# Optimization experiments

Measured on AMD Instinct MI355X. Metric: run time of the kernel, lower is better.

Reference implementation:

```python
import jax, jax.numpy as jnp
import numpy as np

N = 100000   # nodes
E = 800000   # edges (avg degree ~8)
G = 64       # graphs in batch
F_IN = 64
H = 128
C = 4


def setup_inputs() -> dict:
    key = jax.random.key(0)
    ks = jax.random.split(key, 14)
    def w(k, fin, fout):
        return jax.random.normal(k, (fin, fout), dtype=jnp.float32) * (1.0 / np.sqrt(fin))
    inp = {
        "x": jax.random.normal(ks[0], (N, F_IN), dtype=jnp.float32),
        "W1": w(ks[1], F_IN, H), "b1": jnp.zeros((H,), jnp.float32),
        "W2": w(ks[2], H, H),    "b2": jnp.zeros((H,), jnp.float32),
        "W3": w(ks[3], H, H),    "b3": jnp.zeros((H,), jnp.float32),
        "fw1": w(ks[4], H, H),   "fb1": jnp.zeros((H,), jnp.float32),
        "fw2": w(ks[5], H, C),   "fb2": jnp.zeros((C,), jnp.float32),
        "edge_index": jax.random.randint(ks[6], (2, E), 0, N, dtype=jnp.int32),
        "batch": jnp.sort(jax.random.randint(ks[7], (N,), 0, G, dtype=jnp.int32)),
    }
    return inp


def gcn_conv(x, W, b, src, dst):
    """PyG GCNConv: linear transform, add self-loops, symmetric deg^-1/2 norm, scatter-add."""
    h = x @ W                                                    # [N, H]
    deg = jax.ops.segment_sum(jnp.ones((E,), x.dtype), dst, num_segments=N) + 1.0  # self-loop
    dinv = jax.lax.rsqrt(deg)                                    # [N]
    norm = dinv[src] * dinv[dst]                                 # [E]
    agg = jax.ops.segment_sum(h[src] * norm[:, None], dst, num_segments=N)
    agg = agg + h * (dinv * dinv)[:, None]                       # self-loop term (norm = 1/deg)
    return agg + b


def reference(x, W1, b1, W2, b2, W3, b3, fw1, fb1, fw2, fb2, edge_index, batch):
    src, dst = edge_index[0], edge_index[1]
    h = jax.nn.relu(gcn_conv(x, W1, b1, src, dst))
    h = jax.nn.relu(gcn_conv(h, W2, b2, src, dst))
    h = gcn_conv(h, W3, b3, src, dst)
    # global mean pool over graphs
    s = jax.ops.segment_sum(h, batch, num_segments=G)            # [G, H]
    cnt = jax.ops.segment_sum(jnp.ones((N,), h.dtype), batch, num_segments=G)
    pooled = s / jnp.maximum(cnt, 1.0)[:, None]
    z = jax.nn.relu(pooled @ fw1 + fb1)
    return z @ fw2 + fb2                                          # [G, C]
```

## Files before the change

### kernel.cpp

```cpp
#include <hip/hip_runtime.h>

#define N_NODES 100000
#define N_EDGES 800000
#define G_GRAPHS 64
#define F_INPUT 64
#define H_DIM 128
#define C_OUT 4
#define CSR_CAP 32
#define EDGE_BLOCKS (N_EDGES / 256)
#define CONV_BLOCKS ((N_NODES + 255) / 256)
#define WPACK_BLOCKS 20
#define FILL_SEG 4
#define FILL_CHUNKS 250
#define FILL_RANGE (N_NODES / FILL_SEG)
#define FILL_CHUNK (N_EDGES / FILL_CHUNKS)
#define FILL_BLOCKS (FILL_SEG * FILL_CHUNKS)
#define SEG_SPAN (FILL_RANGE * CSR_CAP)

typedef __attribute__((ext_vector_type(8))) short bf16x8;
typedef __attribute__((ext_vector_type(8))) unsigned short u16x8;
typedef __attribute__((ext_vector_type(4))) float f32x4;

__device__ inline unsigned short f2bf(float f) {
    union { float f; unsigned int u; } v; v.f = f;
    unsigned int u = v.u + 0x7FFFu + ((v.u >> 16) & 1u);
    return (unsigned short)(u >> 16);
}
__device__ inline float bf2f(unsigned short b) {
    union { unsigned int u; float f; } v; v.u = ((unsigned int)b) << 16;
    return v.f;
}
__device__ inline float2 unpack_pair(unsigned int u) {
    union { unsigned int u; float f; } a, b;
    a.u = u << 16; b.u = u & 0xFFFF0000u;
    float2 r; r.x = a.f; r.y = b.f; return r;
}
__device__ inline unsigned char f2fp8(float v) {
    int r = __builtin_amdgcn_cvt_pk_fp8_f32(v, 0.0f, 0, false);
    return (unsigned char)(r & 0xFF);
}

__device__ inline void wpack_one(const float* __restrict__ W, unsigned short* __restrict__ hi,
                                 unsigned short* __restrict__ lo, int K, int t)
{
    int lane = t & 63;
    int tile = t >> 6;
    int KS = K / 32;
    int ct = tile / KS, ks = tile % KS;
    int n  = ct * 16 + (lane & 15);
    int k0 = ks * 32 + (lane >> 4) * 8;
    #pragma unroll
    for (int j = 0; j < 8; j++) {
        float w = W[(k0 + j) * H_DIM + n];
        unsigned short h = f2bf(w);
        hi[t * 8 + j] = h;
        lo[t * 8 + j] = f2bf(w - bf2f(h));
    }
}

__global__ __launch_bounds__(256) void hist_kernel(
    const int* __restrict__ dst, int* __restrict__ cnt, int* __restrict__ paddr,
    const float* __restrict__ W1, const float* __restrict__ W2, const float* __restrict__ W3,
    unsigned short* __restrict__ w1hi, unsigned short* __restrict__ w1lo,
    unsigned short* __restrict__ w2hi, unsigned short* __restrict__ w2lo,
    unsigned short* __restrict__ w3hi, unsigned short* __restrict__ w3lo)
{
    int b = blockIdx.x;
    if (b < EDGE_BLOCKS) {
        int e = b * 256 + threadIdx.x;
        int d = dst[e];
        int sl = atomicAdd(&cnt[d], 1);
        paddr[e] = (sl < CSR_CAP) ? d * CSR_CAP + sl : -1;
        return;
    }
    b -= EDGE_BLOCKS;
    int t = b * 256 + threadIdx.x;
    if (t < 1024)       wpack_one(W1, w1hi, w1lo, F_INPUT, t);
    else if (t < 3072)  wpack_one(W2, w2hi, w2lo, H_DIM, t - 1024);
    else                wpack_one(W3, w3hi, w3lo, H_DIM, t - 3072);
}

__global__ __launch_bounds__(256) void prep_kernel(
    const int* __restrict__ paddr, const int* __restrict__ src,
    int* __restrict__ csr,
    const int* __restrict__ cnti, const float4* __restrict__ x4,
    float* __restrict__ dinv, unsigned int* __restrict__ xb_u,
    unsigned int* __restrict__ p1z, unsigned int* __restrict__ p3z)
{
    int b = blockIdx.x;
    if (b < FILL_BLOCKS) {
        const int r   = b & (FILL_SEG - 1);
        const int m   = b >> 2;
        const int plo = r * SEG_SPAN;
        const int phi = plo + SEG_SPAN;
        const int e0  = m * FILL_CHUNK;
        for (int e = e0 + threadIdx.x; e < e0 + FILL_CHUNK; e += 256) {
            int pa = paddr[e];
            if (pa >= plo && pa < phi)
                csr[pa] = src[e];
        }
        return;
    }
    b -= FILL_BLOCKS;
    __shared__ float dl[256];
    int i = b * 256 + threadIdx.x;
    float dv = 0.0f;
    if (i < N_NODES) {
        int c  = cnti[i];
        int dc = min(c, CSR_CAP);
        dv = rsqrtf((float)c + 1.0f);
        dinv[i] = dv;
        int pad = (dc + 7) & ~7;
        for (int s2 = dc; s2 < pad; s2++)
            csr[(size_t)i * CSR_CAP + s2] = N_NODES;
    } else if (i == N_NODES) {
        for (int c = 0; c < 32; c++) {
            xb_u[(size_t)N_NODES * 32 + c] = 0u;
            p1z [(size_t)N_NODES * 32 + c] = 0u;
            p3z [(size_t)N_NODES * 32 + c] = 0u;
        }
    }
    dl[threadIdx.x] = dv;
    __syncthreads();
    const int row_base = b * 256;
    for (int c = threadIdx.x; c < 256 * 16; c += 256) {
        int r = c >> 4;
        int row = row_base + r;
        if (row < N_NODES) {
            float d2 = dl[r];
            float4 v = x4[(size_t)row * 16 + (c & 15)];
            size_t o = ((size_t)row * 16 + (c & 15)) * 2;
            xb_u[o + 0] = (unsigned int)f2bf(v.x * d2) | ((unsigned int)f2bf(v.y * d2) << 16);
            xb_u[o + 1] = (unsigned int)f2bf(v.z * d2) | ((unsigned int)f2bf(v.w * d2) << 16);
        }
    }
}

__global__ __launch_bounds__(256) void gather1_kernel(
    const unsigned int* __restrict__ xb_u, const int* __restrict__ cnti,
    const int* __restrict__ csr, const float* __restrict__ dinv,
    unsigned int* __restrict__ outb)
{
    int idx = blockIdx.x * 256 + threadIdx.x;
    int i  = idx >> 5;
    int f2 = idx & 31;
    int dc = min(cnti[i], CSR_CAP);
    int beg  = i * CSR_CAP;
    int end8 = beg + ((dc + 7) & ~7);
    float2 acc = unpack_pair(xb_u[(size_t)i * 32 + f2]);
    for (int e = beg; e < end8; e += 8) {
        int4 c0 = *(const int4*)(csr + e);
        int4 c1 = *(const int4*)(csr + e + 4);
        float2 v0 = unpack_pair(xb_u[(size_t)c0.x * 32 + f2]);
        float2 v1 = unpack_pair(xb_u[(size_t)c0.y * 32 + f2]);
        float2 v2 = unpack_pair(xb_u[(size_t)c0.z * 32 + f2]);
        float2 v3 = unpack_pair(xb_u[(size_t)c0.w * 32 + f2]);
        float2 v4 = unpack_pair(xb_u[(size_t)c1.x * 32 + f2]);
        float2 v5 = unpack_pair(xb_u[(size_t)c1.y * 32 + f2]);
        float2 v6 = unpack_pair(xb_u[(size_t)c1.z * 32 + f2]);
        float2 v7 = unpack_pair(xb_u[(size_t)c1.w * 32 + f2]);
        acc.x += ((v0.x + v1.x) + (v2.x + v3.x)) + ((v4.x + v5.x) + (v6.x + v7.x));
        acc.y += ((v0.y + v1.y) + (v2.y + v3.y)) + ((v4.y + v5.y) + (v6.y + v7.y));
    }
    float dv = dinv[i];
    outb[idx] = (unsigned int)f2bf(acc.x * dv) | ((unsigned int)f2bf(acc.y * dv) << 16);
}

__device__ inline void acc_u2(uint2 w, float* __restrict__ a) {
    auto l0 = __builtin_amdgcn_cvt_pk_f32_fp8(w.x, false);
    auto h0 = __builtin_amdgcn_cvt_pk_f32_fp8(w.x, true);
    auto l1 = __builtin_amdgcn_cvt_pk_f32_fp8(w.y, false);
    auto h1 = __builtin_amdgcn_cvt_pk_f32_fp8(w.y, true);
    a[0] += l0[0]; a[1] += l0[1]; a[2] += h0[0]; a[3] += h0[1];
    a[4] += l1[0]; a[5] += l1[1]; a[6] += h1[0]; a[7] += h1[1];
}
__device__ inline void gather_fp8_u2(
    const uint2* __restrict__ base, const int* __restrict__ csr,
    int i, int beg, int end8, float* __restrict__ a)
{
    acc_u2(base[(size_t)i * 16], a);
    for (int e = beg; e < end8; e += 8) {
        int4 c0 = *(const int4*)(csr + e);
        int4 c1 = *(const int4*)(csr + e + 4);
        uint2 w0 = base[(size_t)c0.x * 16];
        uint2 w1 = base[(size_t)c0.y * 16];
        uint2 w2 = base[(size_t)c0.z * 16];
        uint2 w3 = base[(size_t)c0.w * 16];
        uint2 w4 = base[(size_t)c1.x * 16];
        uint2 w5 = base[(size_t)c1.y * 16];
        uint2 w6 = base[(size_t)c1.z * 16];
        uint2 w7 = base[(size_t)c1.w * 16];
        acc_u2(w0, a); acc_u2(w1, a); acc_u2(w2, a); acc_u2(w3, a);
        acc_u2(w4, a); acc_u2(w5, a); acc_u2(w6, a); acc_u2(w7, a);
    }
}

__global__ __launch_bounds__(256) void gather2_kernel(
    const uint2* __restrict__ hs8, const int* __restrict__ cnti,
    const int* __restrict__ csr, const float* __restrict__ dinv,
    const float* __restrict__ bias, uint2* __restrict__ out8)
{
    int idx = blockIdx.x * 256 + threadIdx.x;
    int i  = idx >> 4;
    int f8 = idx & 15;
    int dc = min(cnti[i], CSR_CAP);
    int beg  = i * CSR_CAP;
    int end8 = beg + ((dc + 7) & ~7);
    float a[8] = {0, 0, 0, 0, 0, 0, 0, 0};
    gather_fp8_u2(hs8 + f8, csr, i, beg, end8, a);
    float dv = dinv[i];
    float4 b0 = *(const float4*)(bias + f8 * 8);
    float4 b1 = *(const float4*)(bias + f8 * 8 + 4);
    float v0 = fmaxf(a[0] * dv + b0.x, 0.0f);
    float v1 = fmaxf(a[1] * dv + b0.y, 0.0f);
    float v2 = fmaxf(a[2] * dv + b0.z, 0.0f);
    float v3 = fmaxf(a[3] * dv + b0.w, 0.0f);
    float v4 = fmaxf(a[4] * dv + b1.x, 0.0f);
    float v5 = fmaxf(a[5] * dv + b1.y, 0.0f);
    float v6 = fmaxf(a[6] * dv + b1.z, 0.0f);
    float v7 = fmaxf(a[7] * dv + b1.w, 0.0f);
    int d0 = __builtin_amdgcn_cvt_pk_fp8_f32(v0, v1, 0, false);
    d0 = __builtin_amdgcn_cvt_pk_fp8_f32(v2, v3, d0, true);
    int d1 = __builtin_amdgcn_cvt_pk_fp8_f32(v4, v5, 0, false);
    d1 = __builtin_amdgcn_cvt_pk_fp8_f32(v6, v7, d1, true);
    uint2 o; o.x = (unsigned int)d0; o.y = (unsigned int)d1;
    out8[(size_t)i * 16 + f8] = o;
}

__global__ __launch_bounds__(256) void gather3_kernel(
    const uint2* __restrict__ hs8, const int* __restrict__ cnti,
    const int* __restrict__ csr, const float* __restrict__ dinv,
    const float* __restrict__ bias, uint4* __restrict__ outb)
{
    int idx = blockIdx.x * 256 + threadIdx.x;
    int i  = idx >> 4;
    int f8 = idx & 15;
    int dc = min(cnti[i], CSR_CAP);
    int beg  = i * CSR_CAP;
    int end8 = beg + ((dc + 7) & ~7);
    float a[8] = {0, 0, 0, 0, 0, 0, 0, 0};
    gather_fp8_u2(hs8 + f8, csr, i, beg, end8, a);
    float dv = dinv[i];
    float4 b0 = *(const float4*)(bias + f8 * 8);
    float4 b1 = *(const float4*)(bias + f8 * 8 + 4);
    uint4 o;
    o.x = (unsigned int)f2bf(a[0] * dv + b0.x) | ((unsigned int)f2bf(a[1] * dv + b0.y) << 16);
    o.y = (unsigned int)f2bf(a[2] * dv + b0.z) | ((unsigned int)f2bf(a[3] * dv + b0.w) << 16);
    o.z = (unsigned int)f2bf(a[4] * dv + b1.x) | ((unsigned int)f2bf(a[5] * dv + b1.y) << 16);
    o.w = (unsigned int)f2bf(a[6] * dv + b1.z) | ((unsigned int)f2bf(a[7] * dv + b1.w) << 16);
    outb[(size_t)i * 16 + f8] = o;
}

template <int K, bool BIAS_RELU, bool IN_FP8>
__global__ __launch_bounds__(256) void mfma_gemm_kernel(
    const void* __restrict__ inv, const unsigned short* __restrict__ whi,
    const unsigned short* __restrict__ wlo, const float* __restrict__ dinv,
    const float* __restrict__ bias, unsigned char* __restrict__ out8)
{
    constexpr int KS = K / 32;
    __shared__ unsigned short As[128 * K];

    const int tid  = threadIdx.x;
    const int row0 = blockIdx.x * 128;

    const int CH = 128 * K / 8;
    for (int c = tid; c < CH; c += 256) {
        int mt   = c / (KS * 64);
        int rest = c % (KS * 64);
        int ks   = rest / 64;
        int ln   = rest % 64;
        int r    = mt * 16 + (ln & 15);
        int k    = ks * 32 + (ln >> 4) * 8;
        int gr   = row0 + r; if (gr >= N_NODES) gr = N_NODES - 1;
        if constexpr (IN_FP8) {
            const unsigned char* in8 = (const unsigned char*)inv;
            uint2 t = *(const uint2*)(in8 + (size_t)gr * K + k);
            auto f0 = __builtin_amdgcn_cvt_pk_f32_fp8(t.x, false);
            auto f1 = __builtin_amdgcn_cvt_pk_f32_fp8(t.x, true);
            auto f2 = __builtin_amdgcn_cvt_pk_f32_fp8(t.y, false);
            auto f3 = __builtin_amdgcn_cvt_pk_f32_fp8(t.y, true);
            unsigned int* Au = (unsigned int*)(As + c * 8);
            Au[0] = (unsigned int)f2bf(f0[0]) | ((unsigned int)f2bf(f0[1]) << 16);
            Au[1] = (unsigned int)f2bf(f1[0]) | ((unsigned int)f2bf(f1[1]) << 16);
            Au[2] = (unsigned int)f2bf(f2[0]) | ((unsigned int)f2bf(f2[1]) << 16);
            Au[3] = (unsigned int)f2bf(f3[0]) | ((unsigned int)f2bf(f3[1]) << 16);
        } else {
            const unsigned short* in16 = (const unsigned short*)inv;
            *(u16x8*)(As + c * 8) = *(const u16x8*)(in16 + (size_t)gr * K + k);
        }
    }
    __syncthreads();

    const int w = tid >> 6, lane = tid & 63;
    const int quad = lane >> 4, l16 = lane & 15;

    f32x4 acc[2][8];
    #pragma unroll
    for (int rt = 0; rt < 2; rt++)
        #pragma unroll
        for (int ct = 0; ct < 8; ct++) acc[rt][ct] = (f32x4)(0.0f);

    #pragma unroll
    for (int ks = 0; ks < KS; ks++) {
        bf16x8 a0 = *(const bf16x8*)(As + (((w * 2 + 0) * KS + ks) * 64 + lane) * 8);
        bf16x8 a1 = *(const bf16x8*)(As + (((w * 2 + 1) * KS + ks) * 64 + lane) * 8);
        bf16x8 bh[8], bl[8];
        #pragma unroll
        for (int ct = 0; ct < 8; ct++) {
            bh[ct] = *(const bf16x8*)(whi + ((size_t)(ct * KS + ks) * 64 + lane) * 8);
            bl[ct] = *(const bf16x8*)(wlo + ((size_t)(ct * KS + ks) * 64 + lane) * 8);
        }
        #pragma unroll
        for (int ct = 0; ct < 8; ct++) {
            acc[0][ct] = __builtin_amdgcn_mfma_f32_16x16x32_bf16(a0, bh[ct], acc[0][ct], 0, 0, 0);
            acc[0][ct] = __builtin_amdgcn_mfma_f32_16x16x32_bf16(a0, bl[ct], acc[0][ct], 0, 0, 0);
            acc[1][ct] = __builtin_amdgcn_mfma_f32_16x16x32_bf16(a1, bh[ct], acc[1][ct], 0, 0, 0);
            acc[1][ct] = __builtin_amdgcn_mfma_f32_16x16x32_bf16(a1, bl[ct], acc[1][ct], 0, 0, 0);
        }
    }

    float bv[8];
    if (BIAS_RELU) {
        #pragma unroll
        for (int ct = 0; ct < 8; ct++) bv[ct] = bias[ct * 16 + l16];
    }

    #pragma unroll
    for (int rt = 0; rt < 2; rt++) {
        #pragma unroll
        for (int reg = 0; reg < 4; reg++) {
            int row = row0 + w * 32 + rt * 16 + quad * 4 + reg;
            if (row < N_NODES) {
                float dv = BIAS_RELU ? 0.0f : dinv[row];
                #pragma unroll
                for (int ct = 0; ct < 8; ct++) {
                    float val;
                    if (BIAS_RELU) val = fmaxf(acc[rt][ct][reg] + bv[ct], 0.0f);
                    else           val = acc[rt][ct][reg] * dv;
                    out8[(size_t)row * H_DIM + ct * 16 + l16] = f2fp8(val);
                }
            }
        }
    }
}

__global__ __launch_bounds__(128) void pool_kernel(
    const unsigned short* __restrict__ A, const int* __restrict__ batch,
    float* __restrict__ s, float* __restrict__ cnt)
{
    const int RPB = 32;
    int row0 = blockIdx.x * RPB;
    int f = threadIdx.x;
    int g0 = batch[row0];
    int g1 = batch[row0 + RPB - 1];
    if (g0 == g1) {
        float acc = 0.0f;
        #pragma unroll
        for (int r = 0; r < RPB; r++)
            acc += bf2f(A[(size_t)(row0 + r) * H_DIM + f]);
        unsafeAtomicAdd(&s[g0 * H_DIM + f], acc);
        if (f == 0) unsafeAtomicAdd(&cnt[g0], (float)RPB);
    } else {
        float acc = 0.0f;
        int cur = g0, c = 0;
        for (int r = 0; r < RPB; r++) {
            int g = batch[row0 + r];
            if (g != cur) {
                unsafeAtomicAdd(&s[cur * H_DIM + f], acc);
                if (f == 0) unsafeAtomicAdd(&cnt[cur], (float)c);
                cur = g; acc = 0.0f; c = 0;
            }
            acc += bf2f(A[(size_t)(row0 + r) * H_DIM + f]);
            c++;
        }
        unsafeAtomicAdd(&s[cur * H_DIM + f], acc);
        if (f == 0) unsafeAtomicAdd(&cnt[cur], (float)c);
    }
}

__global__ __launch_bounds__(128) void mlp_kernel(
    const float* __restrict__ s, const float* __restrict__ cnt,
    const float* __restrict__ fw1, const float* __restrict__ fb1,
    const float* __restrict__ fw2, const float* __restrict__ fb2,
    float* __restrict__ out)
{
    __shared__ float p[H_DIM];
    __shared__ float z[H_DIM];
    int g = blockIdx.x;
    int f = threadIdx.x;
    float c = fmaxf(cnt[g], 1.0f);
    p[f] = s[g * H_DIM + f] / c;
    __syncthreads();
    float acc = fb1[f];
    for (int k = 0; k < H_DIM; k++) acc = fmaf(p[k], fw1[k * H_DIM + f], acc);
    z[f] = fmaxf(acc, 0.0f);
    __syncthreads();
    if (f < C_OUT) {
        float o = fb2[f];
        for (int k = 0; k < H_DIM; k++) o = fmaf(z[k], fw2[k * C_OUT + f], o);
        out[g * C_OUT + f] = o;
    }
}

extern "C" void kernel_launch(void* const* d_in, const int* in_sizes, int n_in,
                              void* d_out, int out_size, void* d_ws, size_t ws_size,
                              hipStream_t stream)
{
    const float* x   = (const float*)d_in[0];
    const float* W1  = (const float*)d_in[1];
    const float* b1  = (const float*)d_in[2];
    const float* W2  = (const float*)d_in[3];
    const float* b2  = (const float*)d_in[4];
    const float* W3  = (const float*)d_in[5];
    const float* b3  = (const float*)d_in[6];
    const float* fw1 = (const float*)d_in[7];
    const float* fb1 = (const float*)d_in[8];
    const float* fw2 = (const float*)d_in[9];
    const float* fb2 = (const float*)d_in[10];
    const int*   ei  = (const int*)d_in[11];
    const int*   bat = (const int*)d_in[12];
    const int* esrc = ei;
    const int* edst = ei + N_EDGES;
    float* out = (float*)d_out;

    char* ws = (char*)d_ws;
    unsigned short* xb   = (unsigned short*)ws; ws += (size_t)(N_NODES + 1) * F_INPUT * 2;
    unsigned short* aggA = (unsigned short*)ws; ws += (size_t)N_NODES * F_INPUT * 2;
    unsigned short* aggB = (unsigned short*)ws; ws += (size_t)N_NODES * H_DIM * 2;
    unsigned char*  p0 = (unsigned char*)ws;  ws += (size_t)(N_NODES + 1) * H_DIM;
    unsigned char*  p1 = (unsigned char*)ws;  ws += (size_t)(N_NODES + 1) * H_DIM;
    unsigned char*  p2 = (unsigned char*)ws;  ws += (size_t)(N_NODES + 1) * H_DIM;
    unsigned char*  p3 = (unsigned char*)ws;  ws += (size_t)(N_NODES + 1) * H_DIM;
    unsigned short* w1hi = (unsigned short*)ws; ws += H_DIM * F_INPUT * 2;
    unsigned short* w1lo = (unsigned short*)ws; ws += H_DIM * F_INPUT * 2;
    unsigned short* w2hi = (unsigned short*)ws; ws += H_DIM * H_DIM * 2;
    unsigned short* w2lo = (unsigned short*)ws; ws += H_DIM * H_DIM * 2;
    unsigned short* w3hi = (unsigned short*)ws; ws += H_DIM * H_DIM * 2;
    unsigned short* w3lo = (unsigned short*)ws; ws += H_DIM * H_DIM * 2;
    float* dinv = (float*)ws;  ws += N_NODES * 4;
    int* paddr  = (int*)ws;    ws += (size_t)N_EDGES * 4;
    int* csr    = (int*)ws;    ws += (size_t)N_NODES * CSR_CAP * 4;
    int*   cnti = (int*)ws;    ws += N_NODES * 4;
    float* s    = (float*)ws;  ws += G_GRAPHS * H_DIM * 4;
    float* cnt  = (float*)ws;  ws += G_GRAPHS * 4;

    hipMemsetAsync(cnti, 0, (N_NODES + G_GRAPHS * H_DIM + G_GRAPHS) * sizeof(int), stream);

    hist_kernel<<<EDGE_BLOCKS + WPACK_BLOCKS, 256, 0, stream>>>(
        edst, cnti, paddr, W1, W2, W3, w1hi, w1lo, w2hi, w2lo, w3hi, w3lo);
    prep_kernel<<<FILL_BLOCKS + CONV_BLOCKS, 256, 0, stream>>>(
        paddr, esrc, csr, cnti, (const float4*)x, dinv, (unsigned int*)xb,
        (unsigned int*)p1, (unsigned int*)p3);

    const int gemm_grid = (N_NODES + 127) / 128;

    gather1_kernel<<<(N_NODES * 32) / 256, 256, 0, stream>>>(
        (const unsigned int*)xb, cnti, csr, dinv, (unsigned int*)aggA);
    mfma_gemm_kernel<64, true, false><<<gemm_grid, 256, 0, stream>>>(
        aggA, w1hi, w1lo, dinv, b1, p0);
    mfma_gemm_kernel<128, false, true><<<gemm_grid, 256, 0, stream>>>(
        p0, w2hi, w2lo, dinv, nullptr, p1);
    gather2_kernel<<<(N_NODES * 16) / 256, 256, 0, stream>>>(
        (const uint2*)p1, cnti, csr, dinv, b2, (uint2*)p2);
    mfma_gemm_kernel<128, false, true><<<gemm_grid, 256, 0, stream>>>(
        p2, w3hi, w3lo, dinv, nullptr, p3);
    gather3_kernel<<<(N_NODES * 16) / 256, 256, 0, stream>>>(
        (const uint2*)p3, cnti, csr, dinv, b3, (uint4*)aggB);

    pool_kernel<<<N_NODES / 32, 128, 0, stream>>>(aggB, bat, s, cnt);
    mlp_kernel<<<G_GRAPHS, 128, 0, stream>>>(s, cnt, fw1, fb1, fw2, fb2, out);
}
```

Measured before the change: 308.6 us.

## Fuse layer-2 gather with layer-3 GEMM via shared-memory bf16 tile

```diff
diff --git a/kernel.cpp b/kernel.cpp
--- a/kernel.cpp
+++ b/kernel.cpp
@@ -195,36 +195,77 @@
     }
 }
 
-__global__ __launch_bounds__(256) void gather2_kernel(
+__global__ __launch_bounds__(256) void gemm_g2f_kernel(
     const uint2* __restrict__ hs8, const int* __restrict__ cnti,
     const int* __restrict__ csr, const float* __restrict__ dinv,
-    const float* __restrict__ bias, uint2* __restrict__ out8)
-{
-    int idx = blockIdx.x * 256 + threadIdx.x;
-    int i  = idx >> 4;
-    int f8 = idx & 15;
-    int dc = min(cnti[i], CSR_CAP);
-    int beg  = i * CSR_CAP;
-    int end8 = beg + ((dc + 7) & ~7);
-    float a[8] = {0, 0, 0, 0, 0, 0, 0, 0};
-    gather_fp8_u2(hs8 + f8, csr, i, beg, end8, a);
-    float dv = dinv[i];
-    float4 b0 = *(const float4*)(bias + f8 * 8);
-    float4 b1 = *(const float4*)(bias + f8 * 8 + 4);
-    float v0 = fmaxf(a[0] * dv + b0.x, 0.0f);
-    float v1 = fmaxf(a[1] * dv + b0.y, 0.0f);
-    float v2 = fmaxf(a[2] * dv + b0.z, 0.0f);
-    float v3 = fmaxf(a[3] * dv + b0.w, 0.0f);
-    float v4 = fmaxf(a[4] * dv + b1.x, 0.0f);
-    float v5 = fmaxf(a[5] * dv + b1.y, 0.0f);
-    float v6 = fmaxf(a[6] * dv + b1.z, 0.0f);
-    float v7 = fmaxf(a[7] * dv + b1.w, 0.0f);
-    int d0 = __builtin_amdgcn_cvt_pk_fp8_f32(v0, v1, 0, false);
-    d0 = __builtin_amdgcn_cvt_pk_fp8_f32(v2, v3, d0, true);
-    int d1 = __builtin_amdgcn_cvt_pk_fp8_f32(v4, v5, 0, false);
-    d1 = __builtin_amdgcn_cvt_pk_fp8_f32(v6, v7, d1, true);
-    uint2 o; o.x = (unsigned int)d0; o.y = (unsigned int)d1;
-    out8[(size_t)i * 16 + f8] = o;
+    const unsigned short* __restrict__ whi, const unsigned short* __restrict__ wlo,
+    const float* __restrict__ bias, unsigned char* __restrict__ out8)
+{
+    constexpr int KS = 4;
+    __shared__ unsigned short As[16 * 128];
+    uint4* As4 = (uint4*)As;
+    const int tid  = threadIdx.x;
+    const int row0 = blockIdx.x * 16;
+
+    {
+        int r  = tid >> 4;
+        int f8 = tid & 15;
+        int gr = row0 + r;
+        int dc = min(cnti[gr], CSR_CAP);
+        int beg  = gr * CSR_CAP;
+        int end8 = beg + ((dc + 7) & ~7);
+        float a[8] = {0, 0, 0, 0, 0, 0, 0, 0};
+        gather_fp8_u2(hs8 + f8, csr, gr, beg, end8, a);
+        float dv = dinv[gr];
+        float4 b0 = *(const float4*)(bias + f8 * 8);
+        float4 b1 = *(const float4*)(bias + f8 * 8 + 4);
+        float v0 = fmaxf(a[0] * dv + b0.x, 0.0f);
+        float v1 = fmaxf(a[1] * dv + b0.y, 0.0f);
+        float v2 = fmaxf(a[2] * dv + b0.z, 0.0f);
+        float v3 = fmaxf(a[3] * dv + b0.w, 0.0f);
+        float v4 = fmaxf(a[4] * dv + b1.x, 0.0f);
+        float v5 = fmaxf(a[5] * dv + b1.y, 0.0f);
+        float v6 = fmaxf(a[6] * dv + b1.z, 0.0f);
+        float v7 = fmaxf(a[7] * dv + b1.w, 0.0f);
+        uint4 o;
+        o.x = (unsigned int)f2bf(v0) | ((unsigned int)f2bf(v1) << 16);
+        o.y = (unsigned int)f2bf(v2) | ((unsigned int)f2bf(v3) << 16);
+        o.z = (unsigned int)f2bf(v4) | ((unsigned int)f2bf(v5) << 16);
+        o.w = (unsigned int)f2bf(v6) | ((unsigned int)f2bf(v7) << 16);
+        As4[(f8 >> 2) * 64 + (f8 & 3) * 16 + r] = o;
+    }
+    __syncthreads();
+
+    const int w = tid >> 6, lane = tid & 63;
+    const int quad = lane >> 4, l16 = lane & 15;
+    const int ct0 = w * 2;
+
+    f32x4 acc[2];
+    acc[0] = (f32x4)(0.0f);
+    acc[1] = (f32x4)(0.0f);
+    #pragma unroll
+    for (int ks = 0; ks < KS; ks++) {
+        bf16x8 a0 = *(const bf16x8*)(As + (ks * 64 + lane) * 8);
+        bf16x8 bh[2], bl[2];
+        #pragma unroll
+        for (int c = 0; c < 2; c++) {
+            bh[c] = *(const bf16x8*)(whi + ((size_t)((ct0 + c) * KS + ks) * 64 + lane) * 8);
+            bl[c] = *(const bf16x8*)(wlo + ((size_t)((ct0 + c) * KS + ks) * 64 + lane) * 8);
+        }
+        #pragma unroll
+        for (int c = 0; c < 2; c++) {
+            acc[c] = __builtin_amdgcn_mfma_f32_16x16x32_bf16(a0, bh[c], acc[c], 0, 0, 0);
+            acc[c] = __builtin_amdgcn_mfma_f32_16x16x32_bf16(a0, bl[c], acc[c], 0, 0, 0);
+        }
+    }
+    #pragma unroll
+    for (int reg = 0; reg < 4; reg++) {
+        int row = row0 + quad * 4 + reg;
+        float dvr = dinv[row];
+        #pragma unroll
+        for (int c = 0; c < 2; c++)
+            out8[(size_t)row * H_DIM + (ct0 + c) * 16 + l16] = f2fp8(acc[c][reg] * dvr);
+    }
 }
 
 __global__ __launch_bounds__(256) void gather3_kernel(
@@ -429,7 +470,6 @@
     unsigned short* aggB = (unsigned short*)ws; ws += (size_t)N_NODES * H_DIM * 2;
     unsigned char*  p0 = (unsigned char*)ws;  ws += (size_t)(N_NODES + 1) * H_DIM;
     unsigned char*  p1 = (unsigned char*)ws;  ws += (size_t)(N_NODES + 1) * H_DIM;
-    unsigned char*  p2 = (unsigned char*)ws;  ws += (size_t)(N_NODES + 1) * H_DIM;
     unsigned char*  p3 = (unsigned char*)ws;  ws += (size_t)(N_NODES + 1) * H_DIM;
     unsigned short* w1hi = (unsigned short*)ws; ws += H_DIM * F_INPUT * 2;
     unsigned short* w1lo = (unsigned short*)ws; ws += H_DIM * F_INPUT * 2;
@@ -460,10 +500,8 @@
         aggA, w1hi, w1lo, dinv, b1, p0);
     mfma_gemm_kernel<128, false, true><<<gemm_grid, 256, 0, stream>>>(
         p0, w2hi, w2lo, dinv, nullptr, p1);
-    gather2_kernel<<<(N_NODES * 16) / 256, 256, 0, stream>>>(
-        (const uint2*)p1, cnti, csr, dinv, b2, (uint2*)p2);
-    mfma_gemm_kernel<128, false, true><<<gemm_grid, 256, 0, stream>>>(
-        p2, w3hi, w3lo, dinv, nullptr, p3);
+    gemm_g2f_kernel<<<N_NODES / 16, 256, 0, stream>>>(
+        (const uint2*)p1, cnti, csr, dinv, w3hi, w3lo, b2, p3);
     gather3_kernel<<<(N_NODES * 16) / 256, 256, 0, stream>>>(
         (const uint2*)p3, cnti, csr, dinv, b3, (uint4*)aggB);
 
```

Measured after the change: 302.8 us. About the same (-1.9%).
